# Kernel optimization log

Hardware: AMD Instinct MI355X
Metric: run time of the kernel (lower is better)

## Reference

```python
import jax, jax.numpy as jnp
import numpy as np
import math

B, S, H, NH = 8, 1024, 1024, 16
DH = H // NH


def _ln(x, g, b, eps=1e-5):
    m = x.mean(-1, keepdims=True)
    v = ((x - m) ** 2).mean(-1, keepdims=True)
    return (x - m) / jnp.sqrt(v + eps) * g + b


def _attn(qx, kx, vx, wq, bq, wk, bk, wv, bv, wo, bo, mask):
    b = qx.shape[0]
    def heads(t, w, bias):
        return (t @ w + bias).reshape(b, -1, NH, DH).transpose(0, 2, 1, 3)
    q, k, v = heads(qx, wq, bq), heads(kx, wk, bk), heads(vx, wv, bv)
    corr = jnp.einsum('bhqd,bhkd->bhqk', q, k) / math.sqrt(DH)  # [B,NH,Sq,Sk]
    corr = jnp.where(mask[:, None, :, None] == 0, -1e9, corr)  # mask per query row
    p = jax.nn.softmax(corr, axis=-1)
    o = jnp.einsum('bhqk,bhkd->bhqd', p, v).transpose(0, 2, 1, 3).reshape(b, -1, H)
    return o @ wo + bo


def setup_inputs() -> dict:
    key = jax.random.key(0)
    ks = jax.random.split(key, 16)
    d = {}
    d['x'] = jax.random.normal(ks[0], (B, S, H), jnp.float32)
    d['h'] = jax.random.normal(ks[1], (B, S, H), jnp.float32)
    d['mask'] = jnp.ones((B, S), jnp.int32)
    wnames = ['sa_wq', 'sa_wk', 'sa_wv', 'sa_wo', 'ca_wq', 'ca_wk', 'ca_wv', 'ca_wo', 'ff_w1', 'ff_w2']
    for i, n in enumerate(wnames):
        d[n] = jax.random.normal(ks[2 + i], (H, H), jnp.float32) * 0.02
    for n in ['sa_bq', 'sa_bk', 'sa_bv', 'sa_bo', 'ca_bq', 'ca_bk', 'ca_bv', 'ca_bo', 'ff_b1', 'ff_b2']:
        d[n] = jnp.zeros((H,), jnp.float32)
    for n in ['ln1', 'ln2', 'ln3', 'lnh', 'ff_ln']:
        d[n + '_g'] = jnp.ones((H,), jnp.float32)
        d[n + '_b'] = jnp.zeros((H,), jnp.float32)
    return d


def reference(x, h, mask, ln1_g, ln1_b, ln2_g, ln2_b, ln3_g, ln3_b, lnh_g, lnh_b,
              sa_wq, sa_bq, sa_wk, sa_bk, sa_wv, sa_bv, sa_wo, sa_bo,
              ca_wq, ca_bq, ca_wk, ca_bk, ca_wv, ca_bv, ca_wo, ca_bo,
              ff_w1, ff_b1, ff_w2, ff_b2, ff_ln_g, ff_ln_b):
    # self-attention block (pre-LN, residual)
    xn = _ln(x, ln1_g, ln1_b)
    hidden_in = _attn(xn, xn, xn, sa_wq, sa_bq, sa_wk, sa_bk, sa_wv, sa_bv, sa_wo, sa_bo, mask) + x
    # cross-attention block
    mid_n = _ln(hidden_in, ln2_g, ln2_b)
    hn = _ln(h, lnh_g, lnh_b)
    hidden_mid = _attn(mid_n, hn, hn, ca_wq, ca_bq, ca_wk, ca_bk, ca_wv, ca_bv, ca_wo, ca_bo, mask) + hidden_in
    # position-wise FFN (Conv1d k=1 == pointwise linear) with its own LN+residual
    y = _ln(hidden_mid, ln3_g, ln3_b)
    ff = jax.nn.relu(y @ ff_w1 + ff_b1) @ ff_w2 + ff_b2
    ffo = _ln(ff + y, ff_ln_g, ff_ln_b)
    return ffo + hidden_mid
```

## Files before the change

### kernel.cpp

```cpp
#include <hip/hip_runtime.h>

typedef unsigned short u16;
typedef unsigned int u32;
typedef float f32x4 __attribute__((ext_vector_type(4)));
typedef float f32x16 __attribute__((ext_vector_type(16)));
typedef __bf16 bf16x8 __attribute__((ext_vector_type(8)));

#define MFMA16(a, b, c) __builtin_amdgcn_mfma_f32_16x16x32_bf16(a, b, c, 0, 0, 0)
#define MFMA32(a, b, c) __builtin_amdgcn_mfma_f32_32x32x16_bf16(a, b, c, 0, 0, 0)
#define PLSWAP(x, y) asm volatile("v_permlane32_swap_b32 %0, %1" : "+v"(x), "+v"(y))
#define CFENCE() asm volatile("" ::: "memory")
#define BAR()                         \
    {                                 \
        CFENCE();                     \
        __builtin_amdgcn_s_barrier(); \
        CFENCE();                     \
    }
#define WAITV(n) asm volatile("s_waitcnt vmcnt(" #n ")" ::: "memory")

__device__ __forceinline__ u16 f2b(float f) {
    u32 u = __builtin_bit_cast(u32, f);
    u += 0x7fffu + ((u >> 16) & 1u);
    return (u16)(u >> 16);
}

__device__ __forceinline__ u32 pk2(float a, float b) {
    union { u32 u; __bf16 h[2]; } r;
    r.h[0] = (__bf16)a; r.h[1] = (__bf16)b;
    return r.u;
}

__device__ __forceinline__ void gload16(const u16* g, u16* l) {
    __builtin_amdgcn_global_load_lds((const __attribute__((address_space(1))) void*)g,
                                     (__attribute__((address_space(3))) void*)l, 16, 0, 0);
}

struct W10 { const float* p[10]; };
__global__ __launch_bounds__(256) void tcvt_k(W10 wp, u16* __restrict__ WT0) {
    const float* __restrict__ Wm = wp.p[blockIdx.z];
    u16* __restrict__ WT = WT0 + (size_t)blockIdx.z * 1048576;
    __shared__ float t[32][33];
    int bx = blockIdx.x, by = blockIdx.y;
    int tx = threadIdx.x, ty = threadIdx.y;
#pragma unroll
    for (int j = 0; j < 32; j += 8)
        t[ty + j][tx] = Wm[(size_t)(by * 32 + ty + j) * 1024 + bx * 32 + tx];
    __syncthreads();
#pragma unroll
    for (int j = 0; j < 32; j += 8)
        WT[(size_t)(bx * 32 + ty + j) * 1024 + by * 32 + tx] = f2b(t[tx][ty + j]);
}

__global__ __launch_bounds__(256) void vtr_k(const u16* __restrict__ Vg, int ldv, u16* __restrict__ VT) {
    __shared__ u16 t[32][34];
    int bx = blockIdx.x, by = blockIdx.y, b = blockIdx.z;
    int tx = threadIdx.x, ty = threadIdx.y;
#pragma unroll
    for (int j = 0; j < 32; j += 8)
        t[ty + j][tx] = Vg[(size_t)(b * 1024 + by * 32 + ty + j) * ldv + bx * 32 + tx];
    __syncthreads();
#pragma unroll
    for (int j = 0; j < 32; j += 8)
        VT[(size_t)(b * 1024 + bx * 32 + ty + j) * 1024 + by * 32 + tx] = t[tx][ty + j];
}

template <int MODE>
__global__ __launch_bounds__(256) void ln_k(const float* __restrict__ in1, const float* __restrict__ in2,
                                            const float* __restrict__ gg, const float* __restrict__ bb,
                                            const float* __restrict__ post,
                                            float* __restrict__ of, u16* __restrict__ ob) {
    int row = blockIdx.x, tid = threadIdx.x;
    size_t base = (size_t)row * 1024 + tid * 4;
    float4 x = *(const float4*)(in1 + base);
    if constexpr (MODE & 1) {
        float4 x2 = *(const float4*)(in2 + base);
        x.x += x2.x; x.y += x2.y; x.z += x2.z; x.w += x2.w;
    }
    float s1 = x.x + x.y + x.z + x.w;
    float s2 = x.x * x.x + x.y * x.y + x.z * x.z + x.w * x.w;
#pragma unroll
    for (int m = 32; m >= 1; m >>= 1) { s1 += __shfl_xor(s1, m); s2 += __shfl_xor(s2, m); }
    __shared__ float r1[4], r2[4];
    int lane = tid & 63, w = tid >> 6;
    if (lane == 0) { r1[w] = s1; r2[w] = s2; }
    __syncthreads();
    s1 = r1[0] + r1[1] + r1[2] + r1[3];
    s2 = r2[0] + r2[1] + r2[2] + r2[3];
    float mean = s1 * (1.0f / 1024.0f);
    float var = s2 * (1.0f / 1024.0f) - mean * mean;
    float rstd = rsqrtf(var + 1e-5f);
    float4 gv = *(const float4*)(gg + tid * 4);
    float4 bv = *(const float4*)(bb + tid * 4);
    float y0 = (x.x - mean) * rstd * gv.x + bv.x;
    float y1 = (x.y - mean) * rstd * gv.y + bv.y;
    float y2 = (x.z - mean) * rstd * gv.z + bv.z;
    float y3 = (x.w - mean) * rstd * gv.w + bv.w;
    if constexpr (MODE & 2) {
        float o0 = y0, o1 = y1, o2 = y2, o3 = y3;
        if constexpr (MODE & 8) {
            float4 p = *(const float4*)(post + base);
            o0 += p.x; o1 += p.y; o2 += p.z; o3 += p.w;
        }
        float4 o; o.x = o0; o.y = o1; o.z = o2; o.w = o3;
        *(float4*)(of + base) = o;
    }
    if constexpr (MODE & 4) {
        uint2 pk;
        pk.x = (u32)f2b(y0) | ((u32)f2b(y1) << 16);
        pk.y = (u32)f2b(y2) | ((u32)f2b(y3) << 16);
        *(uint2*)(ob + base) = pk;
    }
}

template <int EPI, int WN, int NBN>
__global__ __launch_bounds__(512) void gemm_k(const u16* __restrict__ A, int lda,
                                              const u16* __restrict__ WT,
                                              const float* __restrict__ b0, const float* __restrict__ b1,
                                              const float* __restrict__ b2,
                                              float sc0, float sc1, float sc2,
                                              const float* __restrict__ res,
                                              void* __restrict__ outp, int ldc) {
    constexpr int ASZ = 8192;
    constexpr int BSZ = (WN == 4) ? 8192 : 4096;
    constexpr int SLOT = ASZ + BSZ;
    constexpr int MR = (WN == 4) ? 8 : 4;
    constexpr int WRS = (WN == 4) ? 128 : 64;
    __shared__ u16 lds[3 * SLOT];
    u16* ldsb = &lds[0];

    int id = blockIdx.x;
    constexpr int NWG = 32 * NBN;
    constexpr int CPX = NWG / 8;
    int swz = (id & 7) * CPX + (id >> 3);
    int bm = swz / NBN, bn = swz % NBN;
    const int m0 = bm * 256, n0 = bn * (WN * 64);
    int tid = threadIdx.x, lane = tid & 63, w = tid >> 6;
    int col = lane & 15, fg = lane >> 4;
    int wr = (WN == 4) ? (w >> 2) : (w >> 1);
    int wc = w & (WN - 1);

    int swzL = ((col * 32) + fg * 8) ^ ((col >> 1) << 3);
    int aoff0 = wr * WRS * 32 + swzL;
    int boff0 = ASZ + wc * 64 * 32 + swzL;

    int r = tid >> 2, g = tid & 3;
    int gr = r ^ ((r >> 3) & 1);
    int gc = g ^ ((r >> 1) & 3);
    const u16* pA = A + (size_t)(m0 + gr) * lda + gc * 8;
    const u16* pB = WT + (size_t)(n0 + gr) * 1024 + gc * 8;

#define STGA(t2, snO)                                                                 \
    {                                                                                 \
        gload16(pA + (size_t)(t2) * 32, ldsb + (snO) + w * 512);                      \
        gload16(pA + (size_t)(t2) * 32 + (size_t)128 * lda, ldsb + (snO) + 4096 + w * 512); \
    }
#define STGB(t2, snO)                                                                 \
    {                                                                                 \
        gload16(pB + (size_t)(t2) * 32, ldsb + (snO) + ASZ + w * 512);                \
        if constexpr (WN == 4) {                                                      \
            gload16(pB + (size_t)(t2) * 32 + (size_t)128 * 1024, ldsb + (snO) + ASZ + 4096 + w * 512); \
        }                                                                             \
    }

    f32x4 acc[MR][4];
#pragma unroll
    for (int m = 0; m < MR; m++)
#pragma unroll
        for (int n = 0; n < 4; n++) acc[m][n] = (f32x4){0.f, 0.f, 0.f, 0.f};

    STGA(0, 0); STGB(0, 0);
    STGA(1, SLOT); STGB(1, SLOT);
    if constexpr (WN == 4) { WAITV(4); } else { WAITV(3); }
    BAR();

    int sc = 0, sn = 2;
    for (int t = 0; t < 32; ++t) {
        int sCur = sc * SLOT, sNxt = sn * SLOT;
        bf16x8 a0[4], bfv[WN];
#pragma unroll
        for (int m = 0; m < 4; m++) a0[m] = *(const bf16x8*)&ldsb[sCur + aoff0 + m * 512];
#pragma unroll
        for (int n = 0; n < WN; n++) bfv[n] = *(const bf16x8*)&ldsb[sCur + boff0 + n * 512];
        if (t < 30) STGA(t + 2, sNxt);
        BAR();
        __builtin_amdgcn_s_setprio(1);
#pragma unroll
        for (int m = 0; m < 4; m++)
#pragma unroll
            for (int n = 0; n < WN; n++) acc[m][n] = MFMA16(a0[m], bfv[n], acc[m][n]);
        __builtin_amdgcn_s_setprio(0);
        BAR();
        if constexpr (WN == 4) {
            bf16x8 a1[4];
#pragma unroll
            for (int m = 0; m < 4; m++) a1[m] = *(const bf16x8*)&ldsb[sCur + aoff0 + (m + 4) * 512];
            if (t < 30) STGB(t + 2, sNxt);
            BAR();
            __builtin_amdgcn_s_setprio(1);
#pragma unroll
            for (int m = 0; m < 4; m++)
#pragma unroll
                for (int n = 0; n < 4; n++) acc[m + 4][n] = MFMA16(a1[m], bfv[n], acc[m + 4][n]);
            __builtin_amdgcn_s_setprio(0);
            if (t < 30) { WAITV(4); } else if (t == 30) { WAITV(0); }
            BAR();
        } else {
            bf16x8 b2[2];
#pragma unroll
            for (int n = 0; n < 2; n++) b2[n] = *(const bf16x8*)&ldsb[sCur + boff0 + (n + 2) * 512];
            if (t < 30) STGB(t + 2, sNxt);
            BAR();
            __builtin_amdgcn_s_setprio(1);
#pragma unroll
            for (int m = 0; m < 4; m++)
#pragma unroll
                for (int n = 0; n < 2; n++) acc[m][n + 2] = MFMA16(a0[m], b2[n], acc[m][n + 2]);
            __builtin_amdgcn_s_setprio(0);
            if (t < 30) { WAITV(3); } else if (t == 30) { WAITV(0); }
            BAR();
        }
        sc = (sc == 2) ? 0 : sc + 1;
        sn = (sn == 2) ? 0 : sn + 1;
    }
#undef STGA
#undef STGB

    int seg = n0 >> 10;
    const float* bp = (seg == 0) ? b0 : (seg == 1 ? b1 : b2);
    float sg = (seg == 0) ? sc0 : (seg == 1 ? sc1 : sc2);
    int nseg = n0 & 1023;
    float bv[4];
#pragma unroll
    for (int n = 0; n < 4; n++) bv[n] = bp[nseg + wc * 64 + n * 16 + col];
#pragma unroll
    for (int m = 0; m < MR; m++) {
#pragma unroll
        for (int rr = 0; rr < 4; rr++) {
            int row = m0 + wr * WRS + m * 16 + fg * 4 + rr;
#pragma unroll
            for (int n = 0; n < 4; n++) {
                int c = n0 + wc * 64 + n * 16 + col;
                size_t idx = (size_t)row * ldc + c;
                float v = (acc[m][n][rr] + bv[n]) * sg;
                if constexpr (EPI == 0) ((u16*)outp)[idx] = f2b(v);
                else if constexpr (EPI == 1) ((u16*)outp)[idx] = f2b(fmaxf(v, 0.f));
                else if constexpr (EPI == 2) ((float*)outp)[idx] = v + res[idx];
            }
        }
    }
}

__global__ __launch_bounds__(512) void attn_k(const u16* __restrict__ Q, int ldq,
                                              const u16* __restrict__ Kc, int ldk,
                                              const u16* __restrict__ VT,
                                              const int* __restrict__ mask,
                                              u16* __restrict__ O, int ldo) {
    const int S = 1024;
    int gid = blockIdx.x;
    int bq = gid >> 7, hh = (gid >> 3) & 15, bb = gid & 7;
    int tid = threadIdx.x, lane = tid & 63, w = tid >> 6;
    int q = lane & 31, hl = lane >> 5;
    int q0w = bq * 256 + w * 32;

    __shared__ u16 sm[18432];
#define KT(b, r, c) sm[(b) * 9216 + (r) * 72 + (c)]
#define VTL(b, r, c) sm[(b) * 9216 + 4608 + (r) * 72 + (c)]

    const u16* Qrow = Q + ((size_t)bb * S + q0w + q) * ldq + hh * 64;
    bool mneg = (mask[bb * S + q0w + q] == 0);
    bf16x8 qf[4];
#pragma unroll
    for (int c = 0; c < 4; c++) {
        qf[c] = *(const bf16x8*)(Qrow + c * 16 + hl * 8);
        if (mneg) qf[c] = (bf16x8)(__bf16)0.f;
    }

    float l = 0.f;
    f32x16 oa[2];
#pragma unroll
    for (int i = 0; i < 16; i++) { oa[0][i] = 0.f; oa[1][i] = 0.f; }

    int kk = tid >> 3, ks = tid & 7;
    const u16* gK = Kc + ((size_t)bb * S + kk) * ldk + hh * 64 + ks * 8;
    const u16* gVT = VT + ((size_t)(bb * 16 + hh) * 64 + kk) * 1024 + ks * 8;
    uint4 kr0, vr0;

#define LOADT(t)                                              \
    {                                                         \
        kr0 = *(const uint4*)(gK + (size_t)(t) * 64 * ldk);   \
        vr0 = *(const uint4*)(gVT + (size_t)(t) * 64);        \
    }
#define STORET(bf)                            \
    {                                         \
        *(uint4*)&KT(bf, kk, ks * 8) = kr0;   \
        *(uint4*)&VTL(bf, kk, ks * 8) = vr0;  \
    }

    LOADT(0);
    STORET(0);

    for (int t = 0; t < 16; ++t) {
        int cur = t & 1;
        if (t < 15) LOADT(t + 1);
        __syncthreads();

        f32x16 sc[2];
#pragma unroll
        for (int i = 0; i < 16; i++) { sc[0][i] = 0.f; sc[1][i] = 0.f; }
        __builtin_amdgcn_s_setprio(1);
#pragma unroll
        for (int st = 0; st < 2; st++)
#pragma unroll
            for (int c = 0; c < 4; c++) {
                bf16x8 kf = *(const bf16x8*)&KT(cur, st * 32 + q, c * 16 + hl * 8);
                sc[st] = MFMA32(kf, qf[c], sc[st]);
            }
        __builtin_amdgcn_s_setprio(0);

#pragma unroll
        for (int st = 0; st < 2; st++)
#pragma unroll
            for (int rr = 0; rr < 16; rr++) sc[st][rr] = exp2f(sc[st][rr]);
        float ts[8];
#pragma unroll
        for (int i = 0; i < 8; i++)
            ts[i] = (sc[0][i] + sc[0][i + 8]) + (sc[1][i] + sc[1][i + 8]);
#pragma unroll
        for (int i = 0; i < 4; i++) ts[i] += ts[i + 4];
        l += (ts[0] + ts[2]) + (ts[1] + ts[3]);

        __builtin_amdgcn_s_setprio(1);
#pragma unroll
        for (int st = 0; st < 2; st++) {
            u32 wv[8];
#pragma unroll
            for (int j = 0; j < 8; j++) wv[j] = pk2(sc[st][2 * j], sc[st][2 * j + 1]);
            PLSWAP(wv[0], wv[2]); PLSWAP(wv[1], wv[3]);
            PLSWAP(wv[4], wv[6]); PLSWAP(wv[5], wv[7]);
#pragma unroll
            for (int c = 0; c < 2; c++) {
                union { u32 u[4]; bf16x8 v; } pb;
                pb.u[0] = wv[c * 4 + 0]; pb.u[1] = wv[c * 4 + 1];
                pb.u[2] = wv[c * 4 + 2]; pb.u[3] = wv[c * 4 + 3];
#pragma unroll
                for (int dd = 0; dd < 2; dd++) {
                    bf16x8 vf = *(const bf16x8*)&VTL(cur, dd * 32 + q, st * 32 + c * 16 + hl * 8);
                    oa[dd] = MFMA32(vf, pb.v, oa[dd]);
                }
            }
        }
        __builtin_amdgcn_s_setprio(0);

        if (t < 15) STORET(cur ^ 1);
    }

    l += __shfl_xor(l, 32);
    __syncthreads();
    float inv = 1.0f / l;
    u16* otw = sm + w * 2304;
#pragma unroll
    for (int dd = 0; dd < 2; dd++)
#pragma unroll
        for (int rr = 0; rr < 16; rr++) {
            int d = (rr & 3) + 8 * (rr >> 2) + 4 * hl + 32 * dd;
            otw[q * 72 + d] = f2b(oa[dd][rr] * inv);
        }
    __syncthreads();
    size_t obase = ((size_t)bb * S + q0w) * ldo + hh * 64;
#pragma unroll
    for (int i = 0; i < 4; i++) {
        int row = i * 8 + (lane >> 3);
        uint4 vdat = *(const uint4*)&otw[row * 72 + (lane & 7) * 8];
        *(uint4*)(O + obase + (size_t)row * ldo + (lane & 7) * 8) = vdat;
    }
#undef KT
#undef VTL
#undef LOADT
#undef STORET
}

extern "C" void kernel_launch(void* const* d_in, const int* in_sizes, int n_in,
                              void* d_out, int out_size, void* d_ws, size_t ws_size,
                              hipStream_t stream) {
    (void)in_sizes; (void)n_in; (void)out_size; (void)ws_size;
    const float* x = (const float*)d_in[0];
    const float* h = (const float*)d_in[1];
    const int* mask = (const int*)d_in[2];
    const float* W[10];
    const float* Bv[10];
    for (int i = 0; i < 10; i++) { W[i] = (const float*)d_in[3 + i]; Bv[i] = (const float*)d_in[13 + i]; }
    const float *ln1g = (const float*)d_in[23], *ln1b = (const float*)d_in[24];
    const float *ln2g = (const float*)d_in[25], *ln2b = (const float*)d_in[26];
    const float *ln3g = (const float*)d_in[27], *ln3b = (const float*)d_in[28];
    const float *lnhg = (const float*)d_in[29], *lnhb = (const float*)d_in[30];
    const float *flng = (const float*)d_in[31], *flnb = (const float*)d_in[32];

    const float SCLE = 0.18033688011112042f;

    char* ws = (char*)d_ws;
    size_t off = 0;
    auto alloc = [&](size_t bytes) -> char* {
        char* p = ws + off;
        off += (bytes + 255) & ~(size_t)255;
        return p;
    };
    const size_t MT = (size_t)8192 * 1024;
    u16* wtb = (u16*)alloc((size_t)10 * 1048576 * 2);
    u16* wt[10];
    for (int i = 0; i < 10; i++) wt[i] = wtb + (size_t)i * 1048576;
    u16* qkv = (u16*)alloc((size_t)8192 * 3072 * 2);
    u16* kv = qkv;
    u16* kb = qkv + (size_t)8192 * 2048;
    u16* bufA = (u16*)alloc(MT * 2);
    u16* qb   = (u16*)alloc(MT * 2);
    float* hid_in  = (float*)alloc(MT * 4);
    float* hid_mid = (float*)alloc(MT * 4);
    float* yf      = (float*)alloc(MT * 4);
    u16* hn = (u16*)yf;
    u16* vt_sa = bufA;
    u16* vt_ca = (u16*)hid_mid;
    float* outF = (float*)d_out;

    W10 wp;
    for (int i = 0; i < 10; i++) wp.p[i] = W[i];
    tcvt_k<<<dim3(32, 32, 10), dim3(32, 8), 0, stream>>>(wp, wtb);

    ln_k<4><<<8192, 256, 0, stream>>>(x, nullptr, ln1g, ln1b, nullptr, nullptr, bufA);
    gemm_k<0, 2, 24><<<768, 512, 0, stream>>>(bufA, 1024, wt[0], Bv[0], Bv[1], Bv[2], SCLE, 1.f, 1.f, nullptr, qkv, 3072);
    vtr_k<<<dim3(32, 32, 8), dim3(32, 8), 0, stream>>>(qkv + 2048, 3072, vt_sa);
    attn_k<<<512, 512, 0, stream>>>(qkv, 3072, qkv + 1024, 3072, vt_sa, mask, qkv, 3072);
    gemm_k<2, 2, 8><<<256, 512, 0, stream>>>(qkv, 3072, wt[3], Bv[3], Bv[3], Bv[3], 1.f, 1.f, 1.f, x, hid_in, 1024);

    ln_k<4><<<8192, 256, 0, stream>>>(hid_in, nullptr, ln2g, ln2b, nullptr, nullptr, bufA);
    ln_k<4><<<8192, 256, 0, stream>>>(h, nullptr, lnhg, lnhb, nullptr, nullptr, hn);
    gemm_k<0, 2, 8><<<256, 512, 0, stream>>>(bufA, 1024, wt[4], Bv[4], Bv[4], Bv[4], SCLE, 1.f, 1.f, nullptr, qb, 1024);
    gemm_k<0, 2, 16><<<512, 512, 0, stream>>>(hn, 1024, wt[5], Bv[5], Bv[6], Bv[6], 1.f, 1.f, 1.f, nullptr, kv, 2048);
    vtr_k<<<dim3(32, 32, 8), dim3(32, 8), 0, stream>>>(kv + 1024, 2048, vt_ca);
    attn_k<<<512, 512, 0, stream>>>(qb, 1024, kv, 2048, vt_ca, mask, qb, 1024);
    gemm_k<2, 2, 8><<<256, 512, 0, stream>>>(qb, 1024, wt[7], Bv[7], Bv[7], Bv[7], 1.f, 1.f, 1.f, hid_in, hid_mid, 1024);

    ln_k<6><<<8192, 256, 0, stream>>>(hid_mid, nullptr, ln3g, ln3b, nullptr, yf, bufA);
    gemm_k<1, 2, 8><<<256, 512, 0, stream>>>(bufA, 1024, wt[8], Bv[8], Bv[8], Bv[8], 1.f, 1.f, 1.f, nullptr, kb, 1024);
    gemm_k<2, 2, 8><<<256, 512, 0, stream>>>(kb, 1024, wt[9], Bv[9], Bv[9], Bv[9], 1.f, 1.f, 1.f, yf, hid_in, 1024);
    ln_k<10><<<8192, 256, 0, stream>>>(hid_in, nullptr, flng, flnb, hid_mid, outF, nullptr);
}
```

Baseline: 447.5 us.

## Add 128x128-tile GEMM for N=1024 projections and wave-per-row LayerNorm

Adds a 256-thread GEMM kernel with 128x128 output tiles, used for the 1024-wide projections (out-proj, cross Q, FFN). It launches 512 workgroups instead of 256 so the CUs are better filled. LayerNorm is rewritten so each wavefront handles one row with 16 elements per lane, removing the LDS reduction and block barrier and using wider stores. The trade-off is less operand reuse per tile in the smaller GEMM.

```diff
diff --git a/kernel.cpp b/kernel.cpp
--- a/kernel.cpp
+++ b/kernel.cpp
@@ -69,57 +69,70 @@
                                             const float* __restrict__ gg, const float* __restrict__ bb,
                                             const float* __restrict__ post,
                                             float* __restrict__ of, u16* __restrict__ ob) {
-    int row = blockIdx.x, tid = threadIdx.x;
-    size_t base = (size_t)row * 1024 + tid * 4;
-    float4 x = *(const float4*)(in1 + base);
+    int tid = threadIdx.x, lane = tid & 63, w = tid >> 6;
+    int row = blockIdx.x * 4 + w;
+    size_t base = (size_t)row * 1024 + lane * 16;
+    float x[16];
+#pragma unroll
+    for (int i = 0; i < 4; i++) *(float4*)&x[i * 4] = *(const float4*)(in1 + base + i * 4);
     if constexpr (MODE & 1) {
-        float4 x2 = *(const float4*)(in2 + base);
-        x.x += x2.x; x.y += x2.y; x.z += x2.z; x.w += x2.w;
-    }
-    float s1 = x.x + x.y + x.z + x.w;
-    float s2 = x.x * x.x + x.y * x.y + x.z * x.z + x.w * x.w;
-#pragma unroll
-    for (int m = 32; m >= 1; m >>= 1) { s1 += __shfl_xor(s1, m); s2 += __shfl_xor(s2, m); }
-    __shared__ float r1[4], r2[4];
-    int lane = tid & 63, w = tid >> 6;
-    if (lane == 0) { r1[w] = s1; r2[w] = s2; }
-    __syncthreads();
-    s1 = r1[0] + r1[1] + r1[2] + r1[3];
-    s2 = r2[0] + r2[1] + r2[2] + r2[3];
+#pragma unroll
+        for (int i = 0; i < 4; i++) {
+            float4 v = *(const float4*)(in2 + base + i * 4);
+            x[i * 4] += v.x; x[i * 4 + 1] += v.y; x[i * 4 + 2] += v.z; x[i * 4 + 3] += v.w;
+        }
+    }
+    float s1 = 0.f, s2 = 0.f;
+#pragma unroll
+    for (int i = 0; i < 16; i++) { s1 += x[i]; s2 += x[i] * x[i]; }
+#pragma unroll
+    for (int m = 1; m <= 32; m <<= 1) { s1 += __shfl_xor(s1, m); s2 += __shfl_xor(s2, m); }
     float mean = s1 * (1.0f / 1024.0f);
     float var = s2 * (1.0f / 1024.0f) - mean * mean;
     float rstd = rsqrtf(var + 1e-5f);
-    float4 gv = *(const float4*)(gg + tid * 4);
-    float4 bv = *(const float4*)(bb + tid * 4);
-    float y0 = (x.x - mean) * rstd * gv.x + bv.x;
-    float y1 = (x.y - mean) * rstd * gv.y + bv.y;
-    float y2 = (x.z - mean) * rstd * gv.z + bv.z;
-    float y3 = (x.w - mean) * rstd * gv.w + bv.w;
+    float y[16];
+#pragma unroll
+    for (int i = 0; i < 4; i++) {
+        float4 gv = *(const float4*)(gg + lane * 16 + i * 4);
+        float4 bv = *(const float4*)(bb + lane * 16 + i * 4);
+        y[i * 4 + 0] = (x[i * 4 + 0] - mean) * rstd * gv.x + bv.x;
+        y[i * 4 + 1] = (x[i * 4 + 1] - mean) * rstd * gv.y + bv.y;
+        y[i * 4 + 2] = (x[i * 4 + 2] - mean) * rstd * gv.z + bv.z;
+        y[i * 4 + 3] = (x[i * 4 + 3] - mean) * rstd * gv.w + bv.w;
+    }
     if constexpr (MODE & 2) {
-        float o0 = y0, o1 = y1, o2 = y2, o3 = y3;
-        if constexpr (MODE & 8) {
-            float4 p = *(const float4*)(post + base);
-            o0 += p.x; o1 += p.y; o2 += p.z; o3 += p.w;
-        }
-        float4 o; o.x = o0; o.y = o1; o.z = o2; o.w = o3;
-        *(float4*)(of + base) = o;
+#pragma unroll
+        for (int i = 0; i < 4; i++) {
+            float4 o;
+            o.x = y[i * 4]; o.y = y[i * 4 + 1]; o.z = y[i * 4 + 2]; o.w = y[i * 4 + 3];
+            if constexpr (MODE & 8) {
+                float4 p = *(const float4*)(post + base + i * 4);
+                o.x += p.x; o.y += p.y; o.z += p.z; o.w += p.w;
+            }
+            *(float4*)(of + base + i * 4) = o;
+        }
     }
     if constexpr (MODE & 4) {
-        uint2 pk;
-        pk.x = (u32)f2b(y0) | ((u32)f2b(y1) << 16);
-        pk.y = (u32)f2b(y2) | ((u32)f2b(y3) << 16);
-        *(uint2*)(ob + base) = pk;
+#pragma unroll
+        for (int i = 0; i < 2; i++) {
+            uint4 pk;
+            pk.x = pk2(y[i * 8 + 0], y[i * 8 + 1]);
+            pk.y = pk2(y[i * 8 + 2], y[i * 8 + 3]);
+            pk.z = pk2(y[i * 8 + 4], y[i * 8 + 5]);
+            pk.w = pk2(y[i * 8 + 6], y[i * 8 + 7]);
+            *(uint4*)(ob + base + i * 8) = pk;
+        }
     }
 }
 
 template <int EPI, int WN, int NBN>
-__global__ __launch_bounds__(512) void gemm_k(const u16* __restrict__ A, int lda,
-                                              const u16* __restrict__ WT,
-                                              const float* __restrict__ b0, const float* __restrict__ b1,
-                                              const float* __restrict__ b2,
-                                              float sc0, float sc1, float sc2,
-                                              const float* __restrict__ res,
-                                              void* __restrict__ outp, int ldc) {
+__global__ __launch_bounds__(512) void gemm512_k(const u16* __restrict__ A, int lda,
+                                                 const u16* __restrict__ WT,
+                                                 const float* __restrict__ b0, const float* __restrict__ b1,
+                                                 const float* __restrict__ b2,
+                                                 float sc0, float sc1, float sc2,
+                                                 const float* __restrict__ res,
+                                                 void* __restrict__ outp, int ldc) {
     constexpr int ASZ = 8192;
     constexpr int BSZ = (WN == 4) ? 8192 : 4096;
     constexpr int SLOT = ASZ + BSZ;
@@ -242,6 +255,114 @@
                 int c = n0 + wc * 64 + n * 16 + col;
                 size_t idx = (size_t)row * ldc + c;
                 float v = (acc[m][n][rr] + bv[n]) * sg;
+                if constexpr (EPI == 0) ((u16*)outp)[idx] = f2b(v);
+                else if constexpr (EPI == 1) ((u16*)outp)[idx] = f2b(fmaxf(v, 0.f));
+                else if constexpr (EPI == 2) ((float*)outp)[idx] = v + res[idx];
+            }
+        }
+    }
+}
+
+template <int EPI, int NBN>
+__global__ __launch_bounds__(256) void gemm256_k(const u16* __restrict__ A, int lda,
+                                                 const u16* __restrict__ WT,
+                                                 const float* __restrict__ b0,
+                                                 float sc0,
+                                                 const float* __restrict__ res,
+                                                 void* __restrict__ outp, int ldc) {
+    constexpr int SLOT = 8192;
+    __shared__ u16 lds[3 * SLOT];
+    int id = blockIdx.x;
+    constexpr int NWG = 64 * NBN;
+    constexpr int CPX = NWG / 8;
+    int swz = (id & 7) * CPX + (id >> 3);
+    int bm = swz / NBN, bn = swz % NBN;
+    const int m0 = bm * 128, n0 = bn * 128;
+    int tid = threadIdx.x, lane = tid & 63, w = tid >> 6;
+    int col = lane & 15, fg = lane >> 4;
+    int wr = w >> 1, wc = w & 1;
+
+    int swzL = ((col * 32) + fg * 8) ^ ((col >> 1) << 3);
+    int aoff0 = wr * 64 * 32 + swzL;
+    int boff0 = 4096 + wc * 64 * 32 + swzL;
+
+    int r = tid >> 2, g = tid & 3;
+    int gr = r ^ ((r >> 3) & 1);
+    int gc = g ^ ((r >> 1) & 3);
+    const u16* pA = A + (size_t)(m0 + gr) * lda + gc * 8;
+    const u16* pB = WT + (size_t)(n0 + gr) * 1024 + gc * 8;
+
+#define STGA(t2, snO)                                                                     \
+    {                                                                                     \
+        gload16(pA + (size_t)(t2) * 32, lds + (snO) + w * 512);                           \
+        gload16(pA + (size_t)(t2) * 32 + (size_t)64 * lda, lds + (snO) + 2048 + w * 512); \
+    }
+#define STGB(t2, snO)                                                                             \
+    {                                                                                             \
+        gload16(pB + (size_t)(t2) * 32, lds + (snO) + 4096 + w * 512);                            \
+        gload16(pB + (size_t)(t2) * 32 + (size_t)64 * 1024, lds + (snO) + 4096 + 2048 + w * 512); \
+    }
+
+    f32x4 acc[4][4];
+#pragma unroll
+    for (int m = 0; m < 4; m++)
+#pragma unroll
+        for (int n = 0; n < 4; n++) acc[m][n] = (f32x4){0.f, 0.f, 0.f, 0.f};
+
+    STGA(0, 0); STGB(0, 0);
+    STGA(1, SLOT); STGB(1, SLOT);
+    WAITV(4);
+    BAR();
+
+    int sc = 0, sn = 2;
+    for (int t = 0; t < 32; ++t) {
+        int sCur = sc * SLOT, sNxt = sn * SLOT;
+        bf16x8 a0[4], bfv[2];
+#pragma unroll
+        for (int m = 0; m < 4; m++) a0[m] = *(const bf16x8*)&lds[sCur + aoff0 + m * 512];
+#pragma unroll
+        for (int n = 0; n < 2; n++) bfv[n] = *(const bf16x8*)&lds[sCur + boff0 + n * 512];
+        if (t < 30) STGA(t + 2, sNxt);
+        BAR();
+        __builtin_amdgcn_s_setprio(1);
+#pragma unroll
+        for (int m = 0; m < 4; m++)
+#pragma unroll
+            for (int n = 0; n < 2; n++) acc[m][n] = MFMA16(a0[m], bfv[n], acc[m][n]);
+        __builtin_amdgcn_s_setprio(0);
+        BAR();
+        bf16x8 b2[2];
+#pragma unroll
+        for (int n = 0; n < 2; n++) b2[n] = *(const bf16x8*)&lds[sCur + boff0 + (n + 2) * 512];
+        if (t < 30) STGB(t + 2, sNxt);
+        BAR();
+        __builtin_amdgcn_s_setprio(1);
+#pragma unroll
+        for (int m = 0; m < 4; m++)
+#pragma unroll
+            for (int n = 0; n < 2; n++) acc[m][n + 2] = MFMA16(a0[m], b2[n], acc[m][n + 2]);
+        __builtin_amdgcn_s_setprio(0);
+        if (t < 30) { WAITV(4); } else if (t == 30) { WAITV(0); }
+        BAR();
+        sc = (sc == 2) ? 0 : sc + 1;
+        sn = (sn == 2) ? 0 : sn + 1;
+    }
+#undef STGA
+#undef STGB
+
+    float bv[4];
+#pragma unroll
+    for (int n = 0; n < 4; n++) bv[n] = b0[(n0 & 1023) + wc * 64 + n * 16 + col];
+#pragma unroll
+    for (int m = 0; m < 4; m++) {
+#pragma unroll
+        for (int rr = 0; rr < 4; rr++) {
+            int row = m0 + wr * 64 + m * 16 + fg * 4 + rr;
+#pragma unroll
+            for (int n = 0; n < 4; n++) {
+                int c = n0 + wc * 64 + n * 16 + col;
+                size_t idx = (size_t)row * ldc + c;
+                float v = (acc[m][n][rr] + bv[n]) * sc0;
                 if constexpr (EPI == 0) ((u16*)outp)[idx] = f2b(v);
                 else if constexpr (EPI == 1) ((u16*)outp)[idx] = f2b(fmaxf(v, 0.f));
                 else if constexpr (EPI == 2) ((float*)outp)[idx] = v + res[idx];
@@ -425,22 +546,22 @@
     for (int i = 0; i < 10; i++) wp.p[i] = W[i];
     tcvt_k<<<dim3(32, 32, 10), dim3(32, 8), 0, stream>>>(wp, wtb);
 
-    ln_k<4><<<8192, 256, 0, stream>>>(x, nullptr, ln1g, ln1b, nullptr, nullptr, bufA);
-    gemm_k<0, 2, 24><<<768, 512, 0, stream>>>(bufA, 1024, wt[0], Bv[0], Bv[1], Bv[2], SCLE, 1.f, 1.f, nullptr, qkv, 3072);
+    ln_k<4><<<2048, 256, 0, stream>>>(x, nullptr, ln1g, ln1b, nullptr, nullptr, bufA);
+    gemm512_k<0, 2, 24><<<768, 512, 0, stream>>>(bufA, 1024, wt[0], Bv[0], Bv[1], Bv[2], SCLE, 1.f, 1.f, nullptr, qkv, 3072);
     vtr_k<<<dim3(32, 32, 8), dim3(32, 8), 0, stream>>>(qkv + 2048, 3072, vt_sa);
     attn_k<<<512, 512, 0, stream>>>(qkv, 3072, qkv + 1024, 3072, vt_sa, mask, qkv, 3072);
-    gemm_k<2, 2, 8><<<256, 512, 0, stream>>>(qkv, 3072, wt[3], Bv[3], Bv[3], Bv[3], 1.f, 1.f, 1.f, x, hid_in, 1024);
-
-    ln_k<4><<<8192, 256, 0, stream>>>(hid_in, nullptr, ln2g, ln2b, nullptr, nullptr, bufA);
-    ln_k<4><<<8192, 256, 0, stream>>>(h, nullptr, lnhg, lnhb, nullptr, nullptr, hn);
-    gemm_k<0, 2, 8><<<256, 512, 0, stream>>>(bufA, 1024, wt[4], Bv[4], Bv[4], Bv[4], SCLE, 1.f, 1.f, nullptr, qb, 1024);
-    gemm_k<0, 2, 16><<<512, 512, 0, stream>>>(hn, 1024, wt[5], Bv[5], Bv[6], Bv[6], 1.f, 1.f, 1.f, nullptr, kv, 2048);
+    gemm256_k<2, 8><<<512, 256, 0, stream>>>(qkv, 3072, wt[3], Bv[3], 1.f, x, hid_in, 1024);
+
+    ln_k<4><<<2048, 256, 0, stream>>>(hid_in, nullptr, ln2g, ln2b, nullptr, nullptr, bufA);
+    ln_k<4><<<2048, 256, 0, stream>>>(h, nullptr, lnhg, lnhb, nullptr, nullptr, hn);
+    gemm256_k<0, 8><<<512, 256, 0, stream>>>(bufA, 1024, wt[4], Bv[4], SCLE, nullptr, qb, 1024);
+    gemm512_k<0, 2, 16><<<512, 512, 0, stream>>>(hn, 1024, wt[5], Bv[5], Bv[6], Bv[6], 1.f, 1.f, 1.f, nullptr, kv, 2048);
     vtr_k<<<dim3(32, 32, 8), dim3(32, 8), 0, stream>>>(kv + 1024, 2048, vt_ca);
     attn_k<<<512, 512, 0, stream>>>(qb, 1024, kv, 2048, vt_ca, mask, qb, 1024);
-    gemm_k<2, 2, 8><<<256, 512, 0, stream>>>(qb, 1024, wt[7], Bv[7], Bv[7], Bv[7], 1.f, 1.f, 1.f, hid_in, hid_mid, 1024);
-
-    ln_k<6><<<8192, 256, 0, stream>>>(hid_mid, nullptr, ln3g, ln3b, nullptr, yf, bufA);
-    gemm_k<1, 2, 8><<<256, 512, 0, stream>>>(bufA, 1024, wt[8], Bv[8], Bv[8], Bv[8], 1.f, 1.f, 1.f, nullptr, kb, 1024);
-    gemm_k<2, 2, 8><<<256, 512, 0, stream>>>(kb, 1024, wt[9], Bv[9], Bv[9], Bv[9], 1.f, 1.f, 1.f, yf, hid_in, 1024);
-    ln_k<10><<<8192, 256, 0, stream>>>(hid_in, nullptr, flng, flnb, hid_mid, outF, nullptr);
-}
+    gemm256_k<2, 8><<<512, 256, 0, stream>>>(qb, 1024, wt[7], Bv[7], 1.f, hid_in, hid_mid, 1024);
+
+    ln_k<6><<<2048, 256, 0, stream>>>(hid_mid, nullptr, ln3g, ln3b, nullptr, yf, bufA);
+    gemm256_k<1, 8><<<512, 256, 0, stream>>>(bufA, 1024, wt[8], Bv[8], 1.f, nullptr, kb, 1024);
+    gemm256_k<2, 8><<<512, 256, 0, stream>>>(kb, 1024, wt[9], Bv[9], 1.f, yf, hid_in, 1024);
+    ln_k<10><<<2048, 256, 0, stream>>>(hid_in, nullptr, flng, flnb, hid_mid, outF, nullptr);
+}
```

Result: slower. 457.3 us (+2.2%).
